# Kernel tuning notes

Measured on AMD Instinct MI355X. Metric: run time of the kernel, lower is better.

The kernel has to match this reference:

```python
import jax, jax.numpy as jnp
import numpy as np

B, S, D, H, E, FF = 8, 512, 768, 12, 8, 3072
HD = D // H

def layernorm(x, g, b, eps=1e-5):
    mu = jnp.mean(x, axis=-1, keepdims=True)
    var = jnp.mean((x - mu) ** 2, axis=-1, keepdims=True)
    return (x - mu) * jax.lax.rsqrt(var + eps) * g + b

def setup_inputs() -> dict:
    key = jax.random.key(0)
    ks = jax.random.split(key, 16)
    sd = lambda n: 1.0 / np.sqrt(n)
    return {
        "x": jax.random.normal(ks[0], (B, S, D), jnp.float32),
        "indexes_list": jax.random.randint(ks[1], (1,), 0, E),
        "ln1_g": jnp.ones((D,), jnp.float32),
        "ln1_b": jnp.zeros((D,), jnp.float32),
        "qkv_w": jax.random.normal(ks[2], (D, 3 * D), jnp.float32) * sd(D),
        "proj_w": jax.random.normal(ks[3], (D, D), jnp.float32) * sd(D),
        "proj_b": jnp.zeros((D,), jnp.float32),
        "ln2_g": jnp.ones((D,), jnp.float32),
        "ln2_b": jnp.zeros((D,), jnp.float32),
        "switch_w": jax.random.normal(ks[4], (D, E), jnp.float32) * sd(D),
        "switch_b": jnp.zeros((E,), jnp.float32),
        "w1": jax.random.normal(ks[5], (E, D, FF), jnp.float32) * sd(D),
        "b1": jnp.zeros((E, FF), jnp.float32),
        "w2": jax.random.normal(ks[6], (E, FF, D), jnp.float32) * sd(FF),
        "b2": jnp.zeros((E, D), jnp.float32),
    }

def reference(x, indexes_list, ln1_g, ln1_b, qkv_w, proj_w, proj_b,
              ln2_g, ln2_b, switch_w, switch_b, w1, b1, w2, b2):
    # --- attention sublayer ---
    h = layernorm(x, ln1_g, ln1_b)
    qkv = (h @ qkv_w).reshape(B, S, 3, H, HD).transpose(2, 0, 3, 1, 4)  # [3,B,H,S,hd]
    q, k, v = qkv[0], qkv[1], qkv[2]
    scale = HD ** -0.5
    attn = jax.nn.softmax(jnp.einsum('bhqd,bhkd->bhqk', q, k) * scale, axis=-1)
    o = jnp.einsum('bhqk,bhkd->bhqd', attn, v).transpose(0, 2, 1, 3).reshape(B, S, D)
    x = x + o @ proj_w + proj_b
    # --- switch MoE sublayer (routes arg ignored, as in original) ---
    h = layernorm(x, ln2_g, ln2_b).reshape(B * S, D)  # [T,D]
    logits = h @ switch_w + switch_b
    routes = jnp.argmax(jax.nn.softmax(logits, axis=-1), axis=-1)  # [T]
    # dense per-expert compute, then select by route (same math as gather/scatter)
    y = jax.nn.gelu(jnp.einsum('td,edf->etf', h, w1) + b1[:, None, :], approximate=False)
    y = jax.nn.gelu(jnp.einsum('etf,efd->etd', y, w2) + b2[:, None, :], approximate=False)
    moe_out = y[routes, jnp.arange(B * S)]  # [T,D]
    return x + moe_out.reshape(B, S, D)
```

## Files before the change

kernel.cpp:

```cpp
#include <hip/hip_runtime.h>
#include <math.h>

#define T_TOK   4096
#define D_MODEL 768
#define H_HEADS 12
#define HDIM    64
#define S_SEQ   512
#define B_BATCH 8
#define E_EXP   8
#define FF_DIM  3072
#define MAX_TILES 40
#define MPAD_MAX  (MAX_TILES * 128)

typedef __attribute__((ext_vector_type(8))) short short8;
typedef __attribute__((ext_vector_type(4))) float floatx4;

__device__ __forceinline__ float gelu_exact(float x) {
    return 0.5f * x * (1.0f + erff(x * 0.7071067811865476f));
}

__device__ __forceinline__ unsigned short f2bf(float f) {
    unsigned int u = __float_as_uint(f);
    u += 0x7fffu + ((u >> 16) & 1u);
    return (unsigned short)(u >> 16);
}
__device__ __forceinline__ float bf2f(unsigned short h) {
    return __uint_as_float(((unsigned int)h) << 16);
}
__device__ __forceinline__ void split_bf(float v, unsigned short& hi, unsigned short& lo) {
    hi = f2bf(v);
    lo = f2bf(v - bf2f(hi));
}

__device__ __forceinline__ void gload16(const void* g, void* l) {
    __builtin_amdgcn_global_load_lds(
        (const __attribute__((address_space(1))) unsigned int*)g,
        (__attribute__((address_space(3))) unsigned int*)l, 16, 0, 0);
}
__device__ __forceinline__ int swz3(int r) { return (r ^ (r >> 2)) & 3; }

__global__ void __launch_bounds__(256) ln_f32(const float* __restrict__ x,
                                              const float* __restrict__ g,
                                              const float* __restrict__ b,
                                              float* __restrict__ out) {
    int row = blockIdx.x;
    const float* xr = x + (size_t)row * D_MODEL;
    int tid = threadIdx.x;
    float v0 = xr[tid], v1 = xr[tid + 256], v2 = xr[tid + 512];
    float s = v0 + v1 + v2;
    float q = v0 * v0 + v1 * v1 + v2 * v2;
    for (int off = 32; off; off >>= 1) {
        s += __shfl_down(s, off);
        q += __shfl_down(q, off);
    }
    __shared__ float rs[4], rq[4], stats[2];
    int wid = tid >> 6, lane = tid & 63;
    if (lane == 0) { rs[wid] = s; rq[wid] = q; }
    __syncthreads();
    if (tid == 0) {
        float ts = rs[0] + rs[1] + rs[2] + rs[3];
        float tq = rq[0] + rq[1] + rq[2] + rq[3];
        float mu = ts * (1.0f / 768.0f);
        float var = tq * (1.0f / 768.0f) - mu * mu;
        stats[0] = mu; stats[1] = rsqrtf(var + 1e-5f);
    }
    __syncthreads();
    float mu = stats[0], rstd = stats[1];
    float* orow = out + (size_t)row * D_MODEL;
    orow[tid]       = (v0 - mu) * rstd * g[tid]       + b[tid];
    orow[tid + 256] = (v1 - mu) * rstd * g[tid + 256] + b[tid + 256];
    orow[tid + 512] = (v2 - mu) * rstd * g[tid + 512] + b[tid + 512];
}

__global__ void __launch_bounds__(256) ln_split(const float* __restrict__ x,
                                                const float* __restrict__ g,
                                                const float* __restrict__ b,
                                                unsigned short* __restrict__ ohi,
                                                unsigned short* __restrict__ olo) {
    int row = blockIdx.x;
    const float* xr = x + (size_t)row * D_MODEL;
    int tid = threadIdx.x;
    float v0 = xr[tid], v1 = xr[tid + 256], v2 = xr[tid + 512];
    float s = v0 + v1 + v2;
    float q = v0 * v0 + v1 * v1 + v2 * v2;
    for (int off = 32; off; off >>= 1) {
        s += __shfl_down(s, off);
        q += __shfl_down(q, off);
    }
    __shared__ float rs[4], rq[4], stats[2];
    int wid = tid >> 6, lane = tid & 63;
    if (lane == 0) { rs[wid] = s; rq[wid] = q; }
    __syncthreads();
    if (tid == 0) {
        float ts = rs[0] + rs[1] + rs[2] + rs[3];
        float tq = rq[0] + rq[1] + rq[2] + rq[3];
        float mu = ts * (1.0f / 768.0f);
        float var = tq * (1.0f / 768.0f) - mu * mu;
        stats[0] = mu; stats[1] = rsqrtf(var + 1e-5f);
    }
    __syncthreads();
    float mu = stats[0], rstd = stats[1];
    unsigned short* hr = ohi + (size_t)row * D_MODEL;
    unsigned short* lr = olo + (size_t)row * D_MODEL;
    float r0 = (v0 - mu) * rstd * g[tid]       + b[tid];
    float r1 = (v1 - mu) * rstd * g[tid + 256] + b[tid + 256];
    float r2 = (v2 - mu) * rstd * g[tid + 512] + b[tid + 512];
    unsigned short hi, lo;
    split_bf(r0, hi, lo); hr[tid] = hi;       lr[tid] = lo;
    split_bf(r1, hi, lo); hr[tid + 256] = hi; lr[tid + 256] = lo;
    split_bf(r2, hi, lo); hr[tid + 512] = hi; lr[tid + 512] = lo;
}

__global__ void __launch_bounds__(256) transpose_bf16(const float* __restrict__ in,
                                                      unsigned short* __restrict__ out,
                                                      int R, int C) {
    __shared__ float t[32][33];
    const float* inb = in + (size_t)blockIdx.z * R * C;
    unsigned short* outb = out + (size_t)blockIdx.z * R * C;
    int c0 = blockIdx.x * 32, r0 = blockIdx.y * 32;
    int tx = threadIdx.x & 31, ty = threadIdx.x >> 5;
#pragma unroll
    for (int rr = 0; rr < 32; rr += 8)
        t[ty + rr][tx] = inb[(size_t)(r0 + ty + rr) * C + c0 + tx];
    __syncthreads();
#pragma unroll
    for (int rr = 0; rr < 32; rr += 8)
        outb[(size_t)(c0 + ty + rr) * R + r0 + tx] = f2bf(t[tx][ty + rr]);
}

__global__ void __launch_bounds__(256) transpose_split(const float* __restrict__ in,
                                                       unsigned short* __restrict__ out_hi,
                                                       unsigned short* __restrict__ out_lo,
                                                       int R, int C) {
    __shared__ float t[32][33];
    int c0 = blockIdx.x * 32, r0 = blockIdx.y * 32;
    int tx = threadIdx.x & 31, ty = threadIdx.x >> 5;
#pragma unroll
    for (int rr = 0; rr < 32; rr += 8)
        t[ty + rr][tx] = in[(size_t)(r0 + ty + rr) * C + c0 + tx];
    __syncthreads();
#pragma unroll
    for (int rr = 0; rr < 32; rr += 8) {
        float v = t[tx][ty + rr];
        unsigned short hi, lo;
        split_bf(v, hi, lo);
        size_t idx = (size_t)(c0 + ty + rr) * R + r0 + tx;
        out_hi[idx] = hi;
        out_lo[idx] = lo;
    }
}

__global__ void __launch_bounds__(256) attn_mfma(const float* __restrict__ qkv,
                                                 unsigned short* __restrict__ ohi,
                                                 unsigned short* __restrict__ olo) {
    __shared__ __align__(16) short Kh[64][72], Kl[64][72];
    __shared__ __align__(16) short Vh[64][72], Vl[64][72];

    int qt = blockIdx.x, hh = blockIdx.y, bb = blockIdx.z;
    int tid = threadIdx.x;
    int lane = tid & 63, wv = tid >> 6;
    int lm = lane & 15, q8 = (lane >> 4) * 8, q4 = (lane >> 4) * 4;
    const size_t rstride = 3 * D_MODEL;
    const float* base = qkv + (size_t)bb * S_SEQ * rstride + hh * HDIM;

    short8 qh[2], ql[2];
    {
        const float* qrow = base + (size_t)(qt * 64 + 16 * wv + lm) * rstride;
#pragma unroll
        for (int ks = 0; ks < 2; ks++) {
            float4 v0 = *(const float4*)(qrow + ks * 32 + q8);
            float4 v1 = *(const float4*)(qrow + ks * 32 + q8 + 4);
            unsigned short h_, l_;
            short8 sh, sl;
            split_bf(v0.x * 0.125f, h_, l_); sh[0] = (short)h_; sl[0] = (short)l_;
            split_bf(v0.y * 0.125f, h_, l_); sh[1] = (short)h_; sl[1] = (short)l_;
            split_bf(v0.z * 0.125f, h_, l_); sh[2] = (short)h_; sl[2] = (short)l_;
            split_bf(v0.w * 0.125f, h_, l_); sh[3] = (short)h_; sl[3] = (short)l_;
            split_bf(v1.x * 0.125f, h_, l_); sh[4] = (short)h_; sl[4] = (short)l_;
            split_bf(v1.y * 0.125f, h_, l_); sh[5] = (short)h_; sl[5] = (short)l_;
            split_bf(v1.z * 0.125f, h_, l_); sh[6] = (short)h_; sl[6] = (short)l_;
            split_bf(v1.w * 0.125f, h_, l_); sh[7] = (short)h_; sl[7] = (short)l_;
            qh[ks] = sh; ql[ks] = sl;
        }
    }

    float m_run[4], l_run[4];
    floatx4 o_acc[4];
#pragma unroll
    for (int i = 0; i < 4; i++) {
        m_run[i] = -1e30f; l_run[i] = 0.f;
        o_acc[i] = (floatx4){0.f, 0.f, 0.f, 0.f};
    }

    int sr = tid >> 2;
    int sc0 = (tid & 3) * 16;

    for (int kt = 0; kt < 8; kt++) {
        __syncthreads();
        {
            const float* krow = base + (size_t)(kt * 64 + sr) * rstride + D_MODEL;
            const float* vrow = krow + D_MODEL;
#pragma unroll
            for (int c = 0; c < 16; c += 4) {
                float4 kv = *(const float4*)(krow + sc0 + c);
                ushort4 h4, l4; unsigned short h_, l_;
                split_bf(kv.x, h_, l_); h4.x = h_; l4.x = l_;
                split_bf(kv.y, h_, l_); h4.y = h_; l4.y = l_;
                split_bf(kv.z, h_, l_); h4.z = h_; l4.z = l_;
                split_bf(kv.w, h_, l_); h4.w = h_; l4.w = l_;
                *(ushort4*)&Kh[sr][sc0 + c] = h4;
                *(ushort4*)&Kl[sr][sc0 + c] = l4;
                float4 vv = *(const float4*)(vrow + sc0 + c);
                split_bf(vv.x, h_, l_); Vh[sc0 + c + 0][sr] = (short)h_; Vl[sc0 + c + 0][sr] = (short)l_;
                split_bf(vv.y, h_, l_); Vh[sc0 + c + 1][sr] = (short)h_; Vl[sc0 + c + 1][sr] = (short)l_;
                split_bf(vv.z, h_, l_); Vh[sc0 + c + 2][sr] = (short)h_; Vl[sc0 + c + 2][sr] = (short)l_;
                split_bf(vv.w, h_, l_); Vh[sc0 + c + 3][sr] = (short)h_; Vl[sc0 + c + 3][sr] = (short)l_;
            }
        }
        __syncthreads();

        floatx4 s_acc[4];
#pragma unroll
        for (int nt = 0; nt < 4; nt++) s_acc[nt] = (floatx4){0.f, 0.f, 0.f, 0.f};
#pragma unroll
        for (int ks = 0; ks < 2; ks++) {
#pragma unroll
            for (int nt = 0; nt < 4; nt++) {
                short8 bh = *(const short8*)&Kh[nt * 16 + lm][ks * 32 + q8];
                short8 bl = *(const short8*)&Kl[nt * 16 + lm][ks * 32 + q8];
                s_acc[nt] = __builtin_amdgcn_mfma_f32_16x16x32_bf16(qh[ks], bh, s_acc[nt], 0, 0, 0);
                s_acc[nt] = __builtin_amdgcn_mfma_f32_16x16x32_bf16(qh[ks], bl, s_acc[nt], 0, 0, 0);
                s_acc[nt] = __builtin_amdgcn_mfma_f32_16x16x32_bf16(ql[ks], bh, s_acc[nt], 0, 0, 0);
            }
        }

        float alpha_r[4];
#pragma unroll
        for (int reg = 0; reg < 4; reg++) {
            float tm = fmaxf(fmaxf(s_acc[0][reg], s_acc[1][reg]),
                             fmaxf(s_acc[2][reg], s_acc[3][reg]));
            tm = fmaxf(tm, __shfl_xor(tm, 1));
            tm = fmaxf(tm, __shfl_xor(tm, 2));
            tm = fmaxf(tm, __shfl_xor(tm, 4));
            tm = fmaxf(tm, __shfl_xor(tm, 8));
            float mn = fmaxf(m_run[reg], tm);
            alpha_r[reg] = __expf(m_run[reg] - mn);
            m_run[reg] = mn;
            float ts = 0.f;
#pragma unroll
            for (int nt = 0; nt < 4; nt++) {
                float pv = __expf(s_acc[nt][reg] - mn);
                s_acc[nt][reg] = pv;
                ts += pv;
            }
            ts += __shfl_xor(ts, 1);
            ts += __shfl_xor(ts, 2);
            ts += __shfl_xor(ts, 4);
            ts += __shfl_xor(ts, 8);
            l_run[reg] = l_run[reg] * alpha_r[reg] + ts;
        }

        __syncthreads();

#pragma unroll
        for (int nt = 0; nt < 4; nt++)
#pragma unroll
            for (int reg = 0; reg < 4; reg++) {
                unsigned short h_, l_;
                split_bf(s_acc[nt][reg], h_, l_);
                Kh[16 * wv + q4 + reg][nt * 16 + lm] = (short)h_;
                Kl[16 * wv + q4 + reg][nt * 16 + lm] = (short)l_;
            }
#pragma unroll
        for (int nt = 0; nt < 4; nt++)
#pragma unroll
            for (int reg = 0; reg < 4; reg++) o_acc[nt][reg] *= alpha_r[reg];

        __syncthreads();

#pragma unroll
        for (int ks = 0; ks < 2; ks++) {
            short8 ph = *(const short8*)&Kh[16 * wv + lm][ks * 32 + q8];
            short8 pl = *(const short8*)&Kl[16 * wv + lm][ks * 32 + q8];
#pragma unroll
            for (int nt = 0; nt < 4; nt++) {
                short8 vh = *(const short8*)&Vh[nt * 16 + lm][ks * 32 + q8];
                short8 vl = *(const short8*)&Vl[nt * 16 + lm][ks * 32 + q8];
                o_acc[nt] = __builtin_amdgcn_mfma_f32_16x16x32_bf16(ph, vh, o_acc[nt], 0, 0, 0);
                o_acc[nt] = __builtin_amdgcn_mfma_f32_16x16x32_bf16(ph, vl, o_acc[nt], 0, 0, 0);
                o_acc[nt] = __builtin_amdgcn_mfma_f32_16x16x32_bf16(pl, vh, o_acc[nt], 0, 0, 0);
            }
        }
    }

    size_t ob = (size_t)(bb * S_SEQ + qt * 64) * D_MODEL + hh * HDIM;
#pragma unroll
    for (int reg = 0; reg < 4; reg++) {
        float inv = 1.0f / l_run[reg];
#pragma unroll
        for (int nt = 0; nt < 4; nt++) {
            unsigned short h_, l_;
            split_bf(o_acc[nt][reg] * inv, h_, l_);
            size_t idx = ob + (size_t)(16 * wv + q4 + reg) * D_MODEL + nt * 16 + lm;
            ohi[idx] = h_;
            olo[idx] = l_;
        }
    }
}

__global__ void __launch_bounds__(64) router_kernel(const float* __restrict__ h2,
                                                    const float* __restrict__ sw,
                                                    const float* __restrict__ sb,
                                                    int* __restrict__ routes,
                                                    int* __restrict__ counts) {
    int t = blockIdx.x;
    int lane = threadIdx.x;
    const float* hr = h2 + (size_t)t * D_MODEL;
    float acc[8] = {};
    for (int d = lane; d < D_MODEL; d += 64) {
        float hv = hr[d];
        const float* wr = sw + (size_t)d * 8;
#pragma unroll
        for (int e = 0; e < 8; e++) acc[e] += hv * wr[e];
    }
#pragma unroll
    for (int e = 0; e < 8; e++)
        for (int off = 32; off; off >>= 1) acc[e] += __shfl_down(acc[e], off);
    if (lane == 0) {
        int best = 0;
        float bv = acc[0] + sb[0];
#pragma unroll
        for (int e = 1; e < 8; e++) {
            float v = acc[e] + sb[e];
            if (v > bv) { bv = v; best = e; }
        }
        routes[t] = best;
        atomicAdd(&counts[best], 1);
    }
}

__global__ void __launch_bounds__(256) init_kernel(int* counts, int* cursor, int* perm) {
    int idx = blockIdx.x * 256 + threadIdx.x;
    if (idx < MPAD_MAX) perm[idx] = -1;
    if (idx < 8) { counts[idx] = 0; cursor[idx] = 0; }
}

__global__ void moe_plan(const int* __restrict__ counts, int* pad_base,
                         int* tile_e, int* tile_row0, int* ntiles) {
    if (threadIdx.x == 0 && blockIdx.x == 0) {
        int base = 0, nt = 0;
        for (int e = 0; e < E_EXP; e++) {
            pad_base[e] = base;
            int c = counts[e];
            int nte = (c + 127) >> 7;
            for (int j = 0; j < nte; j++) {
                tile_e[nt] = e;
                tile_row0[nt] = base + j * 128;
                nt++;
            }
            base += nte * 128;
        }
        ntiles[0] = nt;
    }
}

__global__ void __launch_bounds__(256) scatter_kernel(const int* __restrict__ routes,
                                                      const int* __restrict__ pad_base,
                                                      int* __restrict__ cursor,
                                                      int* __restrict__ perm) {
    int t = blockIdx.x * 256 + threadIdx.x;
    if (t < T_TOK) {
        int e = routes[t];
        int pos = atomicAdd(&cursor[e], 1);
        perm[pad_base[e] + pos] = t;
    }
}

__global__ void __launch_bounds__(256) gather_bf16(const float* __restrict__ h2,
                                                   const int* __restrict__ perm,
                                                   unsigned short* __restrict__ Ag) {
    int g = blockIdx.x;
    int row = perm[g];
    unsigned short* dst = Ag + (size_t)g * D_MODEL;
    if (row >= 0) {
        const float* src = h2 + (size_t)row * D_MODEL;
        for (int d = threadIdx.x; d < D_MODEL; d += 256) dst[d] = f2bf(src[d]);
    } else {
        for (int d = threadIdx.x; d < D_MODEL; d += 256) dst[d] = 0;
    }
}

template <int MODE>
__global__ void __launch_bounds__(256) sgemm(const unsigned short* __restrict__ Ah_,
                                             const unsigned short* __restrict__ Al_,
                                             const unsigned short* __restrict__ Bh_,
                                             const unsigned short* __restrict__ Bl_,
                                             const float* __restrict__ bias,
                                             const float* __restrict__ resid,
                                             float* __restrict__ Cf,
                                             int N, int K) {
    __shared__ __align__(16) short Ah[2][128][32];
    __shared__ __align__(16) short Al[2][128][32];
    __shared__ __align__(16) short Bh[2][128][32];
    __shared__ __align__(16) short Bl[2][128][32];

    int row0 = blockIdx.y * 128, n0 = blockIdx.x * 128;
    int tid = threadIdx.x;
    int lane = tid & 63, wid = tid >> 6;
    int wr0 = (wid >> 1) * 64, wc0 = (wid & 1) * 64;
    int lm = lane & 15, q8 = (lane >> 4) * 8;

    int rch = lane >> 2, sl = lane & 3;
    int rst = wid * 32 + rch;
    int gsb = (sl ^ swz3(rst)) << 4;

    const unsigned short* Ahb = Ah_ + (size_t)row0 * K;
    const unsigned short* Alb = Al_ + (size_t)row0 * K;
    const unsigned short* Bhb = Bh_ + (size_t)n0 * K;
    const unsigned short* Blb = Bl_ + (size_t)n0 * K;

    const char* gAh = (const char*)(Ahb + (size_t)rst * K) + gsb;
    const char* gAl = (const char*)(Alb + (size_t)rst * K) + gsb;
    const char* gBh = (const char*)(Bhb + (size_t)rst * K) + gsb;
    const char* gBl = (const char*)(Blb + (size_t)rst * K) + gsb;
    size_t r16 = (size_t)16 * K * 2;

    auto stage = [&](int b, int t) {
        size_t kb = (size_t)t * 64;
        gload16(gAh + kb,       &Ah[b][wid * 32][0]);
        gload16(gAh + r16 + kb, &Ah[b][wid * 32 + 16][0]);
        gload16(gAl + kb,       &Al[b][wid * 32][0]);
        gload16(gAl + r16 + kb, &Al[b][wid * 32 + 16][0]);
        gload16(gBh + kb,       &Bh[b][wid * 32][0]);
        gload16(gBh + r16 + kb, &Bh[b][wid * 32 + 16][0]);
        gload16(gBl + kb,       &Bl[b][wid * 32][0]);
        gload16(gBl + r16 + kb, &Bl[b][wid * 32 + 16][0]);
    };

    floatx4 acc[4][4];
#pragma unroll
    for (int i = 0; i < 4; i++)
#pragma unroll
        for (int j = 0; j < 4; j++) acc[i][j] = (floatx4){0.f, 0.f, 0.f, 0.f};

    const int NSTEP = K >> 5;
    stage(0, 0);
    __syncthreads();

    int cur = 0;
    for (int t = 0; t < NSTEP; t++) {
        if (t + 1 < NSTEP) stage(cur ^ 1, t + 1);

        short8 ah[4], al[4], bh[4], bl[4];
#pragma unroll
        for (int i = 0; i < 4; i++) {
            int r = wr0 + i * 16 + lm;
            int bo = (q8 * 2) ^ (swz3(r) << 4);
            ah[i] = *(const short8*)((const char*)&Ah[cur][r][0] + bo);
            al[i] = *(const short8*)((const char*)&Al[cur][r][0] + bo);
        }
#pragma unroll
        for (int j = 0; j < 4; j++) {
            int r = wc0 + j * 16 + lm;
            int bo = (q8 * 2) ^ (swz3(r) << 4);
            bh[j] = *(const short8*)((const char*)&Bh[cur][r][0] + bo);
            bl[j] = *(const short8*)((const char*)&Bl[cur][r][0] + bo);
        }
#pragma unroll
        for (int i = 0; i < 4; i++)
#pragma unroll
            for (int j = 0; j < 4; j++) {
                acc[i][j] = __builtin_amdgcn_mfma_f32_16x16x32_bf16(ah[i], bh[j], acc[i][j], 0, 0, 0);
                acc[i][j] = __builtin_amdgcn_mfma_f32_16x16x32_bf16(ah[i], bl[j], acc[i][j], 0, 0, 0);
                acc[i][j] = __builtin_amdgcn_mfma_f32_16x16x32_bf16(al[i], bh[j], acc[i][j], 0, 0, 0);
            }
        __syncthreads();
        cur ^= 1;
    }

    int q4 = (lane >> 4) * 4;
#pragma unroll
    for (int i = 0; i < 4; i++) {
#pragma unroll
        for (int j = 0; j < 4; j++) {
            int c = n0 + wc0 + j * 16 + lm;
#pragma unroll
            for (int reg = 0; reg < 4; reg++) {
                int rloc = wr0 + i * 16 + q4 + reg;
                size_t idx = (size_t)(row0 + rloc) * N + c;
                float v = acc[i][j][reg];
                if constexpr (MODE == 0) Cf[idx] = v;
                else                     Cf[idx] = resid[idx] + v + bias[c];
            }
        }
    }
}

template <int MODE>
__global__ void __launch_bounds__(256) mgemm(const unsigned short* __restrict__ A,
                                             const unsigned short* __restrict__ Bt,
                                             const float* __restrict__ bias,
                                             const float* __restrict__ resid,
                                             float* __restrict__ Cf,
                                             unsigned short* __restrict__ Cb,
                                             int N, int K,
                                             const int* __restrict__ perm,
                                             const int* __restrict__ tile_e,
                                             const int* __restrict__ tile_row0,
                                             const int* __restrict__ ntiles) {
    __shared__ __align__(16) short As[2][128][64];
    __shared__ __align__(16) short Bs[2][128][64];

    if ((int)blockIdx.y >= ntiles[0]) return;
    int e = tile_e[blockIdx.y];
    int row0 = tile_row0[blockIdx.y];
    Bt += (size_t)e * N * K;
    bias += (size_t)e * N;
    int n0 = blockIdx.x * 128;

    int tid = threadIdx.x;
    int lane = tid & 63, wid = tid >> 6;
    int wr0 = (wid >> 1) * 64, wc0 = (wid & 1) * 64;
    int lm = lane & 15, q8 = (lane >> 4) * 8;

    int rl = lane >> 3, sl = lane & 7;
    int gsb = (sl ^ rl) << 4;

    const unsigned short* Abase = A + (size_t)row0 * K;
    const unsigned short* Bbase = Bt + (size_t)n0 * K;
    const char* gA = (const char*)(Abase + (size_t)(wid * 32 + rl) * K) + gsb;
    const char* gB = (const char*)(Bbase + (size_t)(wid * 32 + rl) * K) + gsb;

    auto stage = [&](int b, int t) {
        size_t kb = (size_t)t * 128;
#pragma unroll
        for (int c = 0; c < 4; c++) {
            gload16(gA + (size_t)c * 16 * K + kb, &As[b][wid * 32 + c * 8][0]);
            gload16(gB + (size_t)c * 16 * K + kb, &Bs[b][wid * 32 + c * 8][0]);
        }
    };

    floatx4 acc[4][4];
#pragma unroll
    for (int i = 0; i < 4; i++)
#pragma unroll
        for (int j = 0; j < 4; j++) acc[i][j] = (floatx4){0.f, 0.f, 0.f, 0.f};

    const int NSTEP = K >> 6;
    stage(0, 0);
    __syncthreads();

    int cur = 0;
    for (int t = 0; t < NSTEP; t++) {
        if (t + 1 < NSTEP) stage(cur ^ 1, t + 1);

#pragma unroll
        for (int ks = 0; ks < 2; ks++) {
            short8 af[4], bfr[4];
#pragma unroll
            for (int i = 0; i < 4; i++) {
                int r = wr0 + i * 16 + lm;
                int bo = (ks * 64 + q8 * 2) ^ ((r & 7) << 4);
                af[i] = *(const short8*)((const char*)&As[cur][r][0] + bo);
            }
#pragma unroll
            for (int j = 0; j < 4; j++) {
                int r = wc0 + j * 16 + lm;
                int bo = (ks * 64 + q8 * 2) ^ ((r & 7) << 4);
                bfr[j] = *(const short8*)((const char*)&Bs[cur][r][0] + bo);
            }
#pragma unroll
            for (int i = 0; i < 4; i++)
#pragma unroll
                for (int j = 0; j < 4; j++)
                    acc[i][j] = __builtin_amdgcn_mfma_f32_16x16x32_bf16(af[i], bfr[j], acc[i][j], 0, 0, 0);
        }
        __syncthreads();
        cur ^= 1;
    }

    int q4 = (lane >> 4) * 4;
#pragma unroll
    for (int i = 0; i < 4; i++) {
#pragma unroll
        for (int j = 0; j < 4; j++) {
            int c = n0 + wc0 + j * 16 + lm;
#pragma unroll
            for (int reg = 0; reg < 4; reg++) {
                int rloc = wr0 + i * 16 + q4 + reg;
                float v = acc[i][j][reg];
                if constexpr (MODE == 2) {
                    Cb[(size_t)(row0 + rloc) * N + c] = f2bf(gelu_exact(v + bias[c]));
                } else {
                    int t = perm[row0 + rloc];
                    if (t >= 0) {
                        size_t idx = (size_t)t * N + c;
                        Cf[idx] = resid[idx] + gelu_exact(v + bias[c]);
                    }
                }
            }
        }
    }
}

extern "C" void kernel_launch(void* const* d_in, const int* in_sizes, int n_in,
                              void* d_out, int out_size, void* d_ws, size_t ws_size,
                              hipStream_t stream) {
    const float* x      = (const float*)d_in[0];
    const float* ln1_g  = (const float*)d_in[2];
    const float* ln1_b  = (const float*)d_in[3];
    const float* qkv_w  = (const float*)d_in[4];
    const float* proj_w = (const float*)d_in[5];
    const float* proj_b = (const float*)d_in[6];
    const float* ln2_g  = (const float*)d_in[7];
    const float* ln2_b  = (const float*)d_in[8];
    const float* sw     = (const float*)d_in[9];
    const float* sb     = (const float*)d_in[10];
    const float* w1     = (const float*)d_in[11];
    const float* b1     = (const float*)d_in[12];
    const float* w2     = (const float*)d_in[13];
    const float* b2     = (const float*)d_in[14];
    float* out = (float*)d_out;

    char* p = (char*)d_ws;
    float*          qkv = (float*)p;
    float*          h   = (float*)p;
    unsigned short* y1  = (unsigned short*)p;
    p += (size_t)T_TOK * 2304 * 4;
    unsigned short* h_hi = (unsigned short*)p; p += (size_t)T_TOK * D_MODEL * 2;
    unsigned short* h_lo = (unsigned short*)p; p += (size_t)T_TOK * D_MODEL * 2;
    unsigned short* o_hi = h_hi;
    unsigned short* o_lo = h_lo;
    float* x1 = (float*)p; p += (size_t)T_TOK * D_MODEL * 4;
    unsigned short* Ag     = (unsigned short*)p;
    unsigned short* qwt_hi = (unsigned short*)p;
    unsigned short* qwt_lo = qwt_hi + (size_t)2304 * 768;
    p += (size_t)MPAD_MAX * D_MODEL * 2;
    unsigned short* pwt_hi = (unsigned short*)p; p += (size_t)768 * 768 * 2;
    unsigned short* pwt_lo = (unsigned short*)p; p += (size_t)768 * 768 * 2;
    unsigned short* w1t = (unsigned short*)p; p += (size_t)E_EXP * 3072 * 768 * 2;
    unsigned short* w2t = (unsigned short*)p; p += (size_t)E_EXP * 768 * 3072 * 2;
    int* routes    = (int*)p;
    int* perm      = routes + T_TOK;
    int* counts    = perm + MPAD_MAX;
    int* cursor    = counts + 8;
    int* pad_base  = cursor + 8;
    int* tile_e    = pad_base + 8;
    int* tile_row0 = tile_e + MAX_TILES;
    int* ntiles    = tile_row0 + MAX_TILES;

    transpose_split<<<dim3(2304 / 32, 768 / 32), 256, 0, stream>>>(qkv_w, qwt_hi, qwt_lo, 768, 2304);
    transpose_split<<<dim3(768 / 32, 768 / 32), 256, 0, stream>>>(proj_w, pwt_hi, pwt_lo, 768, 768);
    transpose_bf16<<<dim3(3072 / 32, 768 / 32, 8), 256, 0, stream>>>(w1, w1t, 768, 3072);
    transpose_bf16<<<dim3(768 / 32, 3072 / 32, 8), 256, 0, stream>>>(w2, w2t, 3072, 768);

    ln_split<<<T_TOK, 256, 0, stream>>>(x, ln1_g, ln1_b, h_hi, h_lo);
    sgemm<0><<<dim3(2304 / 128, T_TOK / 128), 256, 0, stream>>>(
        h_hi, h_lo, qwt_hi, qwt_lo, nullptr, nullptr, qkv, 2304, 768);
    attn_mfma<<<dim3(S_SEQ / 64, H_HEADS, B_BATCH), 256, 0, stream>>>(qkv, o_hi, o_lo);
    sgemm<1><<<dim3(768 / 128, T_TOK / 128), 256, 0, stream>>>(
        o_hi, o_lo, pwt_hi, pwt_lo, proj_b, x, x1, 768, 768);
    ln_f32<<<T_TOK, 256, 0, stream>>>(x1, ln2_g, ln2_b, h);
    init_kernel<<<(MPAD_MAX + 255) / 256, 256, 0, stream>>>(counts, cursor, perm);
    router_kernel<<<T_TOK, 64, 0, stream>>>(h, sw, sb, routes, counts);
    moe_plan<<<1, 1, 0, stream>>>(counts, pad_base, tile_e, tile_row0, ntiles);
    scatter_kernel<<<T_TOK / 256, 256, 0, stream>>>(routes, pad_base, cursor, perm);
    gather_bf16<<<MPAD_MAX, 256, 0, stream>>>(h, perm, Ag);
    mgemm<2><<<dim3(FF_DIM / 128, MAX_TILES), 256, 0, stream>>>(
        Ag, w1t, b1, nullptr, nullptr, y1, FF_DIM, 768,
        perm, tile_e, tile_row0, ntiles);
    mgemm<3><<<dim3(D_MODEL / 128, MAX_TILES), 256, 0, stream>>>(
        y1, w2t, b2, x1, out, nullptr, D_MODEL, 3072,
        perm, tile_e, tile_row0, ntiles);
}
```

Measured before the change: 617.0 us.

## Split-K the second MoE expert GEMM with atomic accumulation and separate epilogue

The second expert GEMM (K=3072, N=768) previously launched only 6x~40 blocks. It now splits K four ways across blockIdx.z, and each split atomically adds its partial tile into a zeroed fp32 scratch buffer. A new epilogue kernel then applies bias, GELU and the residual, and scatters rows back by token. This raises block count to fill the GPU, at the cost of zeroing and atomically updating a ~15MB scratch buffer, two extra kernel launches, and nondeterministic summation order.

```diff
diff --git a/kernel.cpp b/kernel.cpp
--- a/kernel.cpp
+++ b/kernel.cpp
@@ -11,6 +11,7 @@
 #define FF_DIM  3072
 #define MAX_TILES 40
 #define MPAD_MAX  (MAX_TILES * 128)
+#define KSPLIT  4
 
 typedef __attribute__((ext_vector_type(8))) short short8;
 typedef __attribute__((ext_vector_type(4))) float floatx4;
@@ -345,6 +346,12 @@
     if (idx < 8) { counts[idx] = 0; cursor[idx] = 0; }
 }
 
+__global__ void __launch_bounds__(256) zero_tmp(float* __restrict__ t) {
+    size_t i = ((size_t)blockIdx.x * 256 + threadIdx.x) * 4;
+    if (i < (size_t)MPAD_MAX * D_MODEL)
+        *(float4*)(t + i) = (float4){0.f, 0.f, 0.f, 0.f};
+}
+
 __global__ void moe_plan(const int* __restrict__ counts, int* pad_base,
                          int* tile_e, int* tile_row0, int* ntiles) {
     if (threadIdx.x == 0 && blockIdx.x == 0) {
@@ -601,6 +608,120 @@
             }
         }
     }
+}
+
+__global__ void __launch_bounds__(256) kgemm(const unsigned short* __restrict__ A,
+                                             const unsigned short* __restrict__ Bt,
+                                             float* __restrict__ tmp,
+                                             int N, int K,
+                                             const int* __restrict__ tile_e,
+                                             const int* __restrict__ tile_row0,
+                                             const int* __restrict__ ntiles) {
+    __shared__ __align__(16) short As[2][128][64];
+    __shared__ __align__(16) short Bs[2][128][64];
+
+    if ((int)blockIdx.y >= ntiles[0]) return;
+    int e = tile_e[blockIdx.y];
+    int row0 = tile_row0[blockIdx.y];
+    Bt += (size_t)e * N * K;
+    int n0 = blockIdx.x * 128;
+    const int KLEN = K / KSPLIT;
+    size_t kbase = (size_t)blockIdx.z * KLEN * 2;
+
+    int tid = threadIdx.x;
+    int lane = tid & 63, wid = tid >> 6;
+    int wr0 = (wid >> 1) * 64, wc0 = (wid & 1) * 64;
+    int lm = lane & 15, q8 = (lane >> 4) * 8;
+
+    int rl = lane >> 3, sl = lane & 7;
+    int gsb = (sl ^ rl) << 4;
+
+    const unsigned short* Abase = A + (size_t)row0 * K;
+    const unsigned short* Bbase = Bt + (size_t)n0 * K;
+    const char* gA = (const char*)(Abase + (size_t)(wid * 32 + rl) * K) + gsb + kbase;
+    const char* gB = (const char*)(Bbase + (size_t)(wid * 32 + rl) * K) + gsb + kbase;
+
+    auto stage = [&](int b, int t) {
+        size_t kb = (size_t)t * 128;
+#pragma unroll
+        for (int c = 0; c < 4; c++) {
+            gload16(gA + (size_t)c * 16 * K + kb, &As[b][wid * 32 + c * 8][0]);
+            gload16(gB + (size_t)c * 16 * K + kb, &Bs[b][wid * 32 + c * 8][0]);
+        }
+    };
+
+    floatx4 acc[4][4];
+#pragma unroll
+    for (int i = 0; i < 4; i++)
+#pragma unroll
+        for (int j = 0; j < 4; j++) acc[i][j] = (floatx4){0.f, 0.f, 0.f, 0.f};
+
+    const int NSTEP = KLEN >> 6;
+    stage(0, 0);
+    __syncthreads();
+
+    int cur = 0;
+    for (int t = 0; t < NSTEP; t++) {
+        if (t + 1 < NSTEP) stage(cur ^ 1, t + 1);
+
+#pragma unroll
+        for (int ks = 0; ks < 2; ks++) {
+            short8 af[4], bfr[4];
+#pragma unroll
+            for (int i = 0; i < 4; i++) {
+                int r = wr0 + i * 16 + lm;
+                int bo = (ks * 64 + q8 * 2) ^ ((r & 7) << 4);
+                af[i] = *(const short8*)((const char*)&As[cur][r][0] + bo);
+            }
+#pragma unroll
+            for (int j = 0; j < 4; j++) {
+                int r = wc0 + j * 16 + lm;
+                int bo = (ks * 64 + q8 * 2) ^ ((r & 7) << 4);
+                bfr[j] = *(const short8*)((const char*)&Bs[cur][r][0] + bo);
+            }
+#pragma unroll
+            for (int i = 0; i < 4; i++)
+#pragma unroll
+                for (int j = 0; j < 4; j++)
+                    acc[i][j] = __builtin_amdgcn_mfma_f32_16x16x32_bf16(af[i], bfr[j], acc[i][j], 0, 0, 0);
+        }
+        __syncthreads();
+        cur ^= 1;
+    }
+
+    int q4 = (lane >> 4) * 4;
+#pragma unroll
+    for (int i = 0; i < 4; i++) {
+#pragma unroll
+        for (int j = 0; j < 4; j++) {
+            int c = n0 + wc0 + j * 16 + lm;
+#pragma unroll
+            for (int reg = 0; reg < 4; reg++) {
+                int rloc = wr0 + i * 16 + q4 + reg;
+                atomicAdd(&tmp[(size_t)(row0 + rloc) * N + c], acc[i][j][reg]);
+            }
+        }
+    }
+}
+
+__global__ void __launch_bounds__(256) moe_epilogue(const float* __restrict__ tmp,
+                                                    const int* __restrict__ perm,
+                                                    const int* __restrict__ routes,
+                                                    const float* __restrict__ b2,
+                                                    const float* __restrict__ x1,
+                                                    float* __restrict__ out) {
+    int g = blockIdx.x;
+    int t = perm[g];
+    if (t < 0) return;
+    int e = routes[t];
+    const float* tr = tmp + (size_t)g * D_MODEL;
+    const float* br = b2 + (size_t)e * D_MODEL;
+    const float* xr = x1 + (size_t)t * D_MODEL;
+    float* orow = out + (size_t)t * D_MODEL;
+    int d = threadIdx.x;
+    orow[d]       = xr[d]       + gelu_exact(tr[d]       + br[d]);
+    orow[d + 256] = xr[d + 256] + gelu_exact(tr[d + 256] + br[d + 256]);
+    orow[d + 512] = xr[d + 512] + gelu_exact(tr[d + 512] + br[d + 512]);
 }
 
 extern "C" void kernel_launch(void* const* d_in, const int* in_sizes, int n_in,
@@ -648,6 +769,9 @@
     int* tile_e    = pad_base + 8;
     int* tile_row0 = tile_e + MAX_TILES;
     int* ntiles    = tile_row0 + MAX_TILES;
+    char* pa = (char*)(ntiles + 1);
+    pa = (char*)(((size_t)pa + 15) & ~(size_t)15);
+    float* tmp = (float*)pa;
 
     transpose_split<<<dim3(2304 / 32, 768 / 32), 256, 0, stream>>>(qkv_w, qwt_hi, qwt_lo, 768, 2304);
     transpose_split<<<dim3(768 / 32, 768 / 32), 256, 0, stream>>>(proj_w, pwt_hi, pwt_lo, 768, 768);
@@ -662,6 +786,7 @@
         o_hi, o_lo, pwt_hi, pwt_lo, proj_b, x, x1, 768, 768);
     ln_f32<<<T_TOK, 256, 0, stream>>>(x1, ln2_g, ln2_b, h);
     init_kernel<<<(MPAD_MAX + 255) / 256, 256, 0, stream>>>(counts, cursor, perm);
+    zero_tmp<<<(MPAD_MAX * D_MODEL / 4 + 255) / 256, 256, 0, stream>>>(tmp);
     router_kernel<<<T_TOK, 64, 0, stream>>>(h, sw, sb, routes, counts);
     moe_plan<<<1, 1, 0, stream>>>(counts, pad_base, tile_e, tile_row0, ntiles);
     scatter_kernel<<<T_TOK / 256, 256, 0, stream>>>(routes, pad_base, cursor, perm);
@@ -669,7 +794,7 @@
     mgemm<2><<<dim3(FF_DIM / 128, MAX_TILES), 256, 0, stream>>>(
         Ag, w1t, b1, nullptr, nullptr, y1, FF_DIM, 768,
         perm, tile_e, tile_row0, ntiles);
-    mgemm<3><<<dim3(D_MODEL / 128, MAX_TILES), 256, 0, stream>>>(
-        y1, w2t, b2, x1, out, nullptr, D_MODEL, 3072,
-        perm, tile_e, tile_row0, ntiles);
-}
+    kgemm<<<dim3(D_MODEL / 128, MAX_TILES, KSPLIT), 256, 0, stream>>>(
+        y1, w2t, tmp, D_MODEL, 3072, tile_e, tile_row0, ntiles);
+    moe_epilogue<<<MPAD_MAX, 256, 0, stream>>>(tmp, perm, routes, b2, x1, out);
+}
```

Measured after the change: 672.8 us. 1.09x slower.
